# Optimization experiments

Measured on AMD Instinct MI355X. Metric: run time of the kernel, lower is better.

The kernel has to match this reference:

```python
import jax, jax.numpy as jnp
import numpy as np

B = 8192
D_IN = 1024
H = 1024
N_LAYERS = 10  # 1 input layer + 9 hidden layers, then output layer H->1


def setup_inputs() -> dict:
    key = jax.random.key(0)
    ks = jax.random.split(key, 7)
    s_in = 1.0 / np.sqrt(D_IN)
    s_h = 1.0 / np.sqrt(H)
    return {
        "x": jax.random.normal(ks[0], (B, D_IN), dtype=jnp.float32),
        "W0": jax.random.normal(ks[1], (H, D_IN), dtype=jnp.float32) * s_in,
        "b0": jax.random.normal(ks[2], (H,), dtype=jnp.float32) * s_in,
        "Wh": jax.random.normal(ks[3], (N_LAYERS - 1, H, H), dtype=jnp.float32) * s_h,
        "bh": jax.random.normal(ks[4], (N_LAYERS - 1, H), dtype=jnp.float32) * s_h,
        "Wout": jax.random.normal(ks[5], (1, H), dtype=jnp.float32) * s_h,
        "bout": jax.random.normal(ks[6], (1,), dtype=jnp.float32) * s_h,
    }


def reference(x, W0, b0, Wh, bh, Wout, bout):
    # First layer: Linear(D_IN -> H) + sigmoid. torch Linear is x @ W.T + b.
    h = jax.nn.sigmoid(x @ W0.T + b0)  # [B, H]

    # Remaining num_layers-1 hidden layers, identical shape -> lax.scan over stacked weights.
    def step(h, wb):
        W, b = wb
        return jax.nn.sigmoid(h @ W.T + b), None

    h, _ = jax.lax.scan(step, h, (Wh, bh))

    # Output layer: Linear(H -> 1), no activation.
    return h @ Wout.T + bout  # [B, 1]
```

## Files before the change

### kernel.cpp

```cpp
#include <hip/hip_runtime.h>
#include <stdint.h>

typedef unsigned short u16;
typedef unsigned int   u32;
typedef _Float16 f16;
typedef __attribute__((ext_vector_type(4))) float    f32x4;
typedef __attribute__((ext_vector_type(8))) _Float16 f16x8;
typedef __attribute__((ext_vector_type(4))) _Float16 f16x4;

#define DIM    1024
#define NROWS  8192
#define NLAYER 10

__device__ __forceinline__ void gl_lds16(const void* g, void* l) {
    __builtin_amdgcn_global_load_lds((const __attribute__((address_space(1))) u32*)g,
                                     (__attribute__((address_space(3))) u32*)l, 16, 0, 0);
}

__global__ __launch_bounds__(256) void conv_weights(const float* __restrict__ W0,
                                                    const float* __restrict__ Wh,
                                                    f16* __restrict__ Wf) {
    int i = (blockIdx.x * 256 + threadIdx.x) * 4;
    const float* src = (i < 1048576) ? (W0 + i) : (Wh + (i - 1048576));
    float4 w = *(const float4*)src;
    f16x4 o;
    o.x = (f16)w.x; o.y = (f16)w.y; o.z = (f16)w.z; o.w = (f16)w.w;
    *(f16x4*)(Wf + i) = o;
}

__global__ __launch_bounds__(256) void conv_x(const float* __restrict__ x,
                                              f16* __restrict__ Af) {
    int i = (blockIdx.x * 256 + threadIdx.x) * 4;
    float4 w = *(const float4*)(x + i);
    f16x4 o;
    o.x = (f16)w.x; o.y = (f16)w.y; o.z = (f16)w.z; o.w = (f16)w.w;
    *(f16x4*)(Af + i) = o;
}

#define ABUF_B 0
#define BBUF_B 32768
#define BUFSZ  49152

__global__ __launch_bounds__(512, 2) void layer_gemm(
        const f16* __restrict__ A,
        const f16* __restrict__ Bg,
        const float* __restrict__ bias,
        f16* __restrict__ O) {
    __shared__ char lds[2 * BUFSZ];

    int bid = blockIdx.x;
    int swz = (bid & 7) * 32 + (bid >> 3);
    int bn = swz & 7;
    int bm = swz >> 3;

    const int tid  = threadIdx.x;
    const int lane = tid & 63;
    const int wid  = tid >> 6;
    const int wr   = wid >> 1;
    const int wc   = wid & 1;

    const int swcol = (((lane & 7) ^ ((lane >> 3) & 7)) << 4);
    const char* gsrc[6];
    u32 ldst[6];
    #pragma unroll
    for (int j = 0; j < 6; ++j) {
        int c = wid * 6 + j;
        if (c < 32) {
            int grow = bm * 256 + c * 8 + (lane >> 3);
            gsrc[j] = (const char*)A + (size_t)grow * 2048 + swcol;
            ldst[j] = ABUF_B + c * 1024;
        } else {
            int c2 = c - 32;
            int grow = bn * 128 + c2 * 8 + (lane >> 3);
            gsrc[j] = (const char*)Bg + (size_t)grow * 2048 + swcol;
            ldst[j] = BBUF_B + c2 * 1024;
        }
    }

    f32x4 acc[4][4];
    #pragma unroll
    for (int mf = 0; mf < 4; ++mf)
        #pragma unroll
        for (int nf = 0; nf < 4; ++nf)
            acc[mf][nf] = (f32x4){0.f, 0.f, 0.f, 0.f};

    #pragma unroll
    for (int j = 0; j < 6; ++j)
        gl_lds16(gsrc[j], (char*)lds + ldst[j]);
    __syncthreads();

    for (int kt = 0; kt < DIM / 64; ++kt) {
        const u32 cb_base = (kt & 1) * BUFSZ;
        if (kt < DIM / 64 - 1) {
            const u32 nb = ((kt + 1) & 1) * BUFSZ;
            #pragma unroll
            for (int j = 0; j < 6; ++j)
                gl_lds16(gsrc[j] + (size_t)(kt + 1) * 128, (char*)lds + nb + ldst[j]);
        }

        #pragma unroll
        for (int ks = 0; ks < 2; ++ks) {
            f16x8 a[4], b[4];
            const int cb = ks * 64 + ((lane >> 4) << 4);
            #pragma unroll
            for (int mf = 0; mf < 4; ++mf) {
                int r = wr * 64 + mf * 16 + (lane & 15);
                int byt = r * 128 + (cb ^ ((r & 7) << 4));
                a[mf] = *(const f16x8*)((const char*)lds + cb_base + ABUF_B + byt);
            }
            #pragma unroll
            for (int nf = 0; nf < 4; ++nf) {
                int r = wc * 64 + nf * 16 + (lane & 15);
                int byt = r * 128 + (cb ^ ((r & 7) << 4));
                b[nf] = *(const f16x8*)((const char*)lds + cb_base + BBUF_B + byt);
            }
            __builtin_amdgcn_s_setprio(1);
            #pragma unroll
            for (int mf = 0; mf < 4; ++mf)
                #pragma unroll
                for (int nf = 0; nf < 4; ++nf)
                    acc[mf][nf] = __builtin_amdgcn_mfma_f32_16x16x32_f16(a[mf], b[nf], acc[mf][nf], 0, 0, 0);
            __builtin_amdgcn_s_setprio(0);
        }
        __syncthreads();
    }

    float bv[4];
    #pragma unroll
    for (int nf = 0; nf < 4; ++nf)
        bv[nf] = bias[bn * 128 + wc * 64 + nf * 16 + (lane & 15)];

    #pragma unroll
    for (int mf = 0; mf < 4; ++mf) {
        #pragma unroll
        for (int nf = 0; nf < 4; ++nf) {
            int gn = bn * 128 + wc * 64 + nf * 16 + (lane & 15);
            #pragma unroll
            for (int j = 0; j < 4; ++j) {
                int gm = bm * 256 + wr * 64 + mf * 16 + ((lane >> 4) << 2) + j;
                float z = acc[mf][nf][j] + bv[nf];
                float h = 1.0f / (1.0f + __expf(-z));
                O[(size_t)gm * DIM + gn] = (f16)h;
            }
        }
    }
}

__global__ __launch_bounds__(256) void out_gemv(const f16* __restrict__ A,
                                                const float* __restrict__ Wout,
                                                const float* __restrict__ bout,
                                                float* __restrict__ out) {
    int wid  = threadIdx.x >> 6;
    int lane = threadIdx.x & 63;
    int row  = blockIdx.x * 4 + wid;
    const f16* p = A + (size_t)row * DIM + lane * 16;
    const float* pw = Wout + lane * 16;
    float s = 0.f;
    #pragma unroll
    for (int i = 0; i < 4; ++i) {
        f16x4 h4 = *(const f16x4*)(p + i * 4);
        float4 w4 = *(const float4*)(pw + i * 4);
        s += (float)h4.x * w4.x + (float)h4.y * w4.y + (float)h4.z * w4.z + (float)h4.w * w4.w;
    }
    #pragma unroll
    for (int off = 32; off > 0; off >>= 1)
        s += __shfl_down(s, off);
    if (lane == 0) out[row] = s + bout[0];
}

extern "C" void kernel_launch(void* const* d_in, const int* in_sizes, int n_in,
                              void* d_out, int out_size, void* d_ws, size_t ws_size,
                              hipStream_t stream) {
    const float* x    = (const float*)d_in[0];
    const float* W0   = (const float*)d_in[1];
    const float* b0   = (const float*)d_in[2];
    const float* Wh   = (const float*)d_in[3];
    const float* bh   = (const float*)d_in[4];
    const float* Wout = (const float*)d_in[5];
    const float* bout = (const float*)d_in[6];
    float* out = (float*)d_out;

    f16* ws = (f16*)d_ws;
    f16* Wf = ws;
    f16* A0 = Wf + (size_t)NLAYER * DIM * DIM;
    f16* A1 = A0 + (size_t)NROWS * DIM;

    conv_weights<<<NLAYER * DIM * DIM / 1024, 256, 0, stream>>>(W0, Wh, Wf);
    conv_x<<<NROWS * DIM / 1024, 256, 0, stream>>>(x, A0);

    const f16* in = A0;
    f16* o = A1;
    for (int l = 0; l < NLAYER; ++l) {
        const float* bias = (l == 0) ? b0 : (bh + (size_t)(l - 1) * DIM);
        layer_gemm<<<256, 512, 0, stream>>>(in, Wf + (size_t)l * DIM * DIM, bias, o);
        f16* t = (f16*)in; in = o; o = t;
    }

    out_gemv<<<NROWS / 4, 256, 0, stream>>>(in, Wout, bout, out);
}
```

Before: 256.8 us.

## Triple-buffer LDS loads with vmcnt waits and vectorize transposed epilogue stores

The K loop moves from double to triple buffering in LDS. It prefetches two stages ahead and uses explicit `s_waitcnt vmcnt` plus one barrier per iteration instead of a full `__syncthreads` at both ends. This aims to hide global-to-LDS load latency behind the MFMA work. The MFMA operands are swapped so each lane holds four consecutive output columns. The epilogue can then load bias as a float4 and write 8-byte packed f16 stores instead of scattered 2-byte stores. LDS use grows to about 144 KB per block, which still fits one block per CU.

Result: slower. 266.4 us (+3.8%).

```diff
diff --git a/kernel.cpp b/kernel.cpp
--- a/kernel.cpp
+++ b/kernel.cpp
@@ -40,13 +40,14 @@
 #define ABUF_B 0
 #define BBUF_B 32768
 #define BUFSZ  49152
+#define NKT    16
 
 __global__ __launch_bounds__(512, 2) void layer_gemm(
         const f16* __restrict__ A,
         const f16* __restrict__ Bg,
         const float* __restrict__ bias,
         f16* __restrict__ O) {
-    __shared__ char lds[2 * BUFSZ];
+    __shared__ char lds[3 * BUFSZ];
 
     int bid = blockIdx.x;
     int swz = (bid & 7) * 32 + (bid >> 3);
@@ -86,18 +87,25 @@
 
     #pragma unroll
     for (int j = 0; j < 6; ++j)
-        gl_lds16(gsrc[j], (char*)lds + ldst[j]);
-    __syncthreads();
-
-    for (int kt = 0; kt < DIM / 64; ++kt) {
-        const u32 cb_base = (kt & 1) * BUFSZ;
-        if (kt < DIM / 64 - 1) {
-            const u32 nb = ((kt + 1) & 1) * BUFSZ;
+        gl_lds16(gsrc[j], lds + ldst[j]);
+    #pragma unroll
+    for (int j = 0; j < 6; ++j)
+        gl_lds16(gsrc[j] + 128, lds + BUFSZ + ldst[j]);
+
+    int cur = 0, nx2 = 2;
+    for (int kt = 0; kt < NKT; ++kt) {
+        if (kt < NKT - 1) asm volatile("s_waitcnt vmcnt(6)" ::: "memory");
+        else              asm volatile("s_waitcnt vmcnt(0)" ::: "memory");
+        __builtin_amdgcn_s_barrier();
+        __builtin_amdgcn_sched_barrier(0);
+
+        if (kt < NKT - 2) {
             #pragma unroll
             for (int j = 0; j < 6; ++j)
-                gl_lds16(gsrc[j] + (size_t)(kt + 1) * 128, (char*)lds + nb + ldst[j]);
-        }
-
+                gl_lds16(gsrc[j] + (size_t)(kt + 2) * 128, lds + nx2 * BUFSZ + ldst[j]);
+        }
+
+        const char* base = lds + cur * BUFSZ;
         #pragma unroll
         for (int ks = 0; ks < 2; ++ks) {
             f16x8 a[4], b[4];
@@ -106,42 +114,40 @@
             for (int mf = 0; mf < 4; ++mf) {
                 int r = wr * 64 + mf * 16 + (lane & 15);
                 int byt = r * 128 + (cb ^ ((r & 7) << 4));
-                a[mf] = *(const f16x8*)((const char*)lds + cb_base + ABUF_B + byt);
+                a[mf] = *(const f16x8*)(base + ABUF_B + byt);
             }
             #pragma unroll
             for (int nf = 0; nf < 4; ++nf) {
                 int r = wc * 64 + nf * 16 + (lane & 15);
                 int byt = r * 128 + (cb ^ ((r & 7) << 4));
-                b[nf] = *(const f16x8*)((const char*)lds + cb_base + BBUF_B + byt);
+                b[nf] = *(const f16x8*)(base + BBUF_B + byt);
             }
             __builtin_amdgcn_s_setprio(1);
             #pragma unroll
             for (int mf = 0; mf < 4; ++mf)
                 #pragma unroll
                 for (int nf = 0; nf < 4; ++nf)
-                    acc[mf][nf] = __builtin_amdgcn_mfma_f32_16x16x32_f16(a[mf], b[nf], acc[mf][nf], 0, 0, 0);
+                    acc[mf][nf] = __builtin_amdgcn_mfma_f32_16x16x32_f16(b[nf], a[mf], acc[mf][nf], 0, 0, 0);
             __builtin_amdgcn_s_setprio(0);
         }
-        __syncthreads();
-    }
-
-    float bv[4];
-    #pragma unroll
-    for (int nf = 0; nf < 4; ++nf)
-        bv[nf] = bias[bn * 128 + wc * 64 + nf * 16 + (lane & 15)];
-
-    #pragma unroll
-    for (int mf = 0; mf < 4; ++mf) {
+        cur = (cur == 2) ? 0 : cur + 1;
+        nx2 = (nx2 == 2) ? 0 : nx2 + 1;
+    }
+
+    #pragma unroll
+    for (int nf = 0; nf < 4; ++nf) {
+        int gn0 = bn * 128 + wc * 64 + nf * 16 + ((lane >> 4) << 2);
+        f32x4 b4 = *(const f32x4*)(bias + gn0);
         #pragma unroll
-        for (int nf = 0; nf < 4; ++nf) {
-            int gn = bn * 128 + wc * 64 + nf * 16 + (lane & 15);
+        for (int mf = 0; mf < 4; ++mf) {
+            int gm = bm * 256 + wr * 64 + mf * 16 + (lane & 15);
+            f16x4 o;
             #pragma unroll
             for (int j = 0; j < 4; ++j) {
-                int gm = bm * 256 + wr * 64 + mf * 16 + ((lane >> 4) << 2) + j;
-                float z = acc[mf][nf][j] + bv[nf];
-                float h = 1.0f / (1.0f + __expf(-z));
-                O[(size_t)gm * DIM + gn] = (f16)h;
+                float z = acc[mf][nf][j] + b4[j];
+                o[j] = (f16)(1.0f / (1.0f + __expf(-z)));
             }
+            *(f16x4*)(O + (size_t)gm * DIM + gn0) = o;
         }
     }
 }
```
